# Performance work log

Measured on AMD Instinct MI355X. Metric: run time of the kernel, lower is better.

The kernel has to match this reference:

```python
import jax, jax.numpy as jnp
import numpy as np

HID, HEADS, HD = 512, 8, 64  # hid_dim, n_heads, head_dim
NEG = -1e10


def setup_inputs() -> dict:
    key = jax.random.key(0)
    ks = jax.random.split(key, 12)
    B, S = 4, 2048
    inp = {
        'query': jax.random.normal(ks[0], (B, S, HID), jnp.float32),
        'key': jax.random.normal(ks[1], (B, S, HID), jnp.float32),
        'value': jax.random.normal(ks[2], (B, S, HID), jnp.float32),
        'mask': jnp.ones((B, 1, 1, S), jnp.int32),
    }
    sc = 1.0 / np.sqrt(HID)
    for i, n in enumerate(['Wq', 'Wk', 'Wv', 'Wo']):
        inp[n] = jax.random.uniform(ks[3 + i], (HID, HID), jnp.float32, -sc, sc)
    for i, n in enumerate(['bq', 'bk', 'bv', 'bo']):
        inp[n] = jax.random.uniform(ks[7 + i], (HID,), jnp.float32, -sc, sc)
    return inp


def reference(query, key, value, mask, Wq, Wk, Wv, Wo, bq, bk, bv, bo):
    B = query.shape[0]

    def proj(x, W, b):
        # torch Linear: x @ W.T + b; then split heads -> [B, H, S, HD]
        y = jnp.einsum('bsd,ed->bse', x, W) + b
        return y.reshape(B, -1, HEADS, HD).transpose(0, 2, 1, 3)

    Q = proj(query, Wq, bq)
    K = proj(key, Wk, bk)
    V = proj(value, Wv, bv)
    scale = jnp.sqrt(jnp.float32(HD))
    E = jnp.einsum('bhqd,bhkd->bhqk', Q, K) / scale  # [B,H,Sq,Sk]
    E = jnp.where(mask == 0, NEG, E)
    A = jax.nn.softmax(E, axis=-1)  # dropout p=0 -> identity
    out = jnp.einsum('bhqk,bhkd->bhqd', A, V)
    out = out.transpose(0, 2, 1, 3).reshape(B, -1, HID)
    return jnp.einsum('bsd,ed->bse', out, Wo) + bo
```

## Files before the change

### kernel.cpp

```cpp
#include <hip/hip_runtime.h>
#include <hip/hip_bf16.h>


typedef __bf16 v8bf __attribute__((ext_vector_type(8)));
typedef __bf16 v4bf __attribute__((ext_vector_type(4)));
typedef float  v4f  __attribute__((ext_vector_type(4)));

#define MFMA16(a, b, c) __builtin_amdgcn_mfma_f32_16x16x32_bf16((a), (b), (c), 0, 0, 0)

__device__ __forceinline__ void gl16(const __bf16* g, __bf16* l) {
    __builtin_amdgcn_global_load_lds(
        (const __attribute__((address_space(1))) void*)g,
        (__attribute__((address_space(3))) void*)l, 16, 0, 0);
}

__device__ inline v8bf cvt8(const float* __restrict__ p) {
    const v4f f0 = *(const v4f*)p;
    const v4f f1 = *(const v4f*)(p + 4);
    v8bf r;
    r[0] = (__bf16)f0[0]; r[1] = (__bf16)f0[1]; r[2] = (__bf16)f0[2]; r[3] = (__bf16)f0[3];
    r[4] = (__bf16)f1[0]; r[5] = (__bf16)f1[1]; r[6] = (__bf16)f1[2]; r[7] = (__bf16)f1[3];
    return r;
}

__global__ __launch_bounds__(256) void cvt_all(
    const float* __restrict__ Wq, const float* __restrict__ Wk,
    const float* __restrict__ Wv, const float* __restrict__ Wo,
    const float* __restrict__ xq, const float* __restrict__ xk,
    const float* __restrict__ xv,
    __bf16* __restrict__ Wb, __bf16* __restrict__ xb)
{
    const int bid = blockIdx.x;
    if (bid < 1024) {
        const int idx = (bid * 256 + threadIdx.x) * 4;
        const int w = idx >> 18, off = idx & 262143;
        const float* src = (w == 0) ? Wq : (w == 1) ? Wk : (w == 2) ? Wv : Wo;
        const v4f x = *(const v4f*)(src + off);
        v4bf y;
        y[0] = (__bf16)x[0]; y[1] = (__bf16)x[1]; y[2] = (__bf16)x[2]; y[3] = (__bf16)x[3];
        *(v4bf*)(Wb + idx) = y;
    } else {
        const int idx = ((bid - 1024) * 256 + threadIdx.x) * 8;
        const int w = idx >> 22, off = idx & 4194303;
        const float* src = (w == 0) ? xq : (w == 1) ? xk : xv;
        *(v8bf*)(xb + idx) = cvt8(src + off);
    }
}

__global__ __launch_bounds__(256) void qkv_gemm(
    const __bf16* __restrict__ xb, const __bf16* __restrict__ Wb,
    const float* __restrict__ bq, const float* __restrict__ bk, const float* __restrict__ bv,
    __bf16* __restrict__ Qo, __bf16* __restrict__ Ko, __bf16* __restrict__ VTo)
{
    const int z = blockIdx.z;
    const __bf16* x    = xb + (size_t)z * 4194304;
    const __bf16* W    = Wb + (size_t)z * 262144;
    const float*  bias = (z == 0) ? bq : (z == 1) ? bk : bv;

    const int tid = threadIdx.x, wave = tid >> 6, lane = tid & 63;
    const int quad = lane >> 4, r = lane & 15;
    const int wm = wave >> 1, wn = wave & 1;
    const int row0 = blockIdx.x * 128, col0 = blockIdx.y * 128;

    __shared__ __align__(16) __bf16 As[2][4096];
    __shared__ __align__(16) __bf16 Bs[2][4096];

    const __bf16* aG[2];
    const __bf16* bG[2];
    int aOff[2];
    for (int j = 0; j < 2; j++) {
        const int s = wave * 2 + j;
        aG[j] = x + (size_t)(row0 + s * 16 + r) * 512 + quad * 8;
        bG[j] = W + (size_t)(col0 + s * 16 + r) * 512 + quad * 8;
        aOff[j] = s * 512;
    }

    v4f acc[4][4] = {};

    for (int j = 0; j < 2; j++) {
        gl16(aG[j], &As[0][aOff[j]]);
        gl16(bG[j], &Bs[0][aOff[j]]);
    }
    __syncthreads();

    for (int t = 0; t < 16; t++) {
        const int cur = t & 1;
        if (t < 15) {
            const int kk = (t + 1) * 32;
            for (int j = 0; j < 2; j++) {
                gl16(aG[j] + kk, &As[cur ^ 1][aOff[j]]);
                gl16(bG[j] + kk, &Bs[cur ^ 1][aOff[j]]);
            }
        }
        v8bf a[4], b[4];
        for (int i = 0; i < 4; i++)
            a[i] = ((const v8bf*)As[cur])[(wm * 4 + i) * 64 + lane];
        for (int i = 0; i < 4; i++)
            b[i] = ((const v8bf*)Bs[cur])[(wn * 4 + i) * 64 + lane];
        for (int mi = 0; mi < 4; mi++)
            for (int ni = 0; ni < 4; ni++)
                acc[mi][ni] = MFMA16(a[mi], b[ni], acc[mi][ni]);
        __syncthreads();
    }

    for (int ni = 0; ni < 4; ni++) {
        const int n = col0 + wn * 64 + ni * 16 + r;
        const float bv_ = bias[n];
        const int hh = n >> 6, hd = n & 63;
        for (int mi = 0; mi < 4; mi++) {
            const int mbase = row0 + wm * 64 + mi * 16 + quad * 4;
            const int bb = mbase >> 11, s0 = mbase & 2047;
            if (z == 2) {
                v4bf pk;
                for (int i = 0; i < 4; i++)
                    pk[i] = (__bf16)(acc[mi][ni][i] + bv_);
                *(v4bf*)&VTo[((size_t)((bb * 8 + hh) * 64 + hd)) * 2048 + s0] = pk;
            } else {
                __bf16* dst = (z == 0) ? Qo : Ko;
                for (int i = 0; i < 4; i++)
                    dst[((size_t)((bb * 8 + hh) * 2048 + s0 + i)) * 64 + hd] =
                        (__bf16)(acc[mi][ni][i] + bv_);
            }
        }
    }
}

__global__ __launch_bounds__(256, 4) void attn(
    const __bf16* __restrict__ Q, const __bf16* __restrict__ K,
    const __bf16* __restrict__ VT, const int* __restrict__ mask,
    float* __restrict__ P0, float* __restrict__ P1,
    float* __restrict__ L0, float* __restrict__ L1)
{
    const int id = blockIdx.y * 16 + blockIdx.x;
    const int x8 = id & 7, j = (id >> 3) & 3, qb = id >> 5;
    const int bh = x8 * 4 + j;
    const int b = bh >> 3, h = bh & 7;
    const int ks = blockIdx.z;
    float* __restrict__ Pp = ks ? P1 : P0;
    float* __restrict__ Lp = ks ? L1 : L0;
    const int tid = threadIdx.x, wave = tid >> 6, lane = tid & 63;
    const int quad = lane >> 4, r = lane & 15;
    const int q0 = qb * 128 + wave * 32;

    const __bf16* Qb = Q  + (size_t)bh * 2048 * 64;
    const __bf16* Kb = K  + (size_t)bh * 2048 * 64 + (size_t)ks * 1024 * 64;
    const __bf16* Vb = VT + (size_t)bh * 64 * 2048 + ks * 1024;
    const int*    mb = mask + (size_t)b * 2048 + ks * 1024;

    __shared__ __align__(16) __bf16 Kls[4096];
    __shared__ __align__(16) __bf16 Vls[4096];
    __shared__ __align__(16) float  biasF[1024];
    __shared__ __align__(16) __bf16 PF[4][4][64][8];

    for (int i = tid; i < 1024; i += 256)
        biasF[i] = (mb[i] != 0) ? 0.f : -1.0e10f;

    const int e1 = tid, e2 = tid + 256;
    int seg, l, t_, h_, rr, qd;
    seg = e1 >> 6; l = e1 & 63; t_ = seg >> 1; h_ = seg & 1; rr = l & 15; qd = l >> 4;
    const __bf16* kg1 = Kb + (size_t)(16 * t_ + rr) * 64   + h_ * 32 + qd * 8;
    const __bf16* vg1 = Vb + (size_t)(16 * t_ + rr) * 2048 + h_ * 32 + qd * 8;
    seg = e2 >> 6; l = e2 & 63; t_ = seg >> 1; h_ = seg & 1; rr = l & 15; qd = l >> 4;
    const __bf16* kg2 = Kb + (size_t)(16 * t_ + rr) * 64   + h_ * 32 + qd * 8;
    const __bf16* vg2 = Vb + (size_t)(16 * t_ + rr) * 2048 + h_ * 32 + qd * 8;

    v8bf qf[2][2];
    for (int g = 0; g < 2; g++) {
        qf[g][0] = *(const v8bf*)(Qb + (size_t)(q0 + g * 16 + r) * 64 +      quad * 8);
        qf[g][1] = *(const v8bf*)(Qb + (size_t)(q0 + g * 16 + r) * 64 + 32 + quad * 8);
    }

    v8bf ones;
    for (int i = 0; i < 8; i++) ones[i] = (__bf16)1.0f;

    v4f o[2][4] = {};
    v4f osum[2] = {};

    const float SC = 0.18033688f;

    const int entE = (quad >> 1) * 16 + r;
    const int entO = entE + 32;
    const int eoff = (quad & 1) * 4;

    v8bf ks1 = *(const v8bf*)kg1, ks2 = *(const v8bf*)kg2;
    v8bf vs1 = *(const v8bf*)vg1, vs2 = *(const v8bf*)vg2;

    for (int t = 0; t < 16; t++) {
        __syncthreads();
        ((v8bf*)Kls)[e1] = ks1; ((v8bf*)Kls)[e2] = ks2;
        ((v8bf*)Vls)[e1] = vs1; ((v8bf*)Vls)[e2] = vs2;
        __syncthreads();
        if (t < 15) {
            const int k0n = (t + 1) * 64;
            ks1 = *(const v8bf*)(kg1 + (size_t)k0n * 64);
            ks2 = *(const v8bf*)(kg2 + (size_t)k0n * 64);
            vs1 = *(const v8bf*)(vg1 + k0n);
            vs2 = *(const v8bf*)(vg2 + k0n);
        }
        const int k0 = t * 64;

        v4f sa[2][4] = {};
        for (int tt = 0; tt < 4; tt++) {
            const v8bf kf0 = ((const v8bf*)Kls)[(tt * 2 + 0) * 64 + lane];
            const v8bf kf1 = ((const v8bf*)Kls)[(tt * 2 + 1) * 64 + lane];
            sa[0][tt] = MFMA16(kf0, qf[0][0], sa[0][tt]);
            sa[0][tt] = MFMA16(kf1, qf[0][1], sa[0][tt]);
            sa[1][tt] = MFMA16(kf0, qf[1][0], sa[1][tt]);
            sa[1][tt] = MFMA16(kf1, qf[1][1], sa[1][tt]);
        }

        for (int tt = 0; tt < 4; tt++) {
            const v4f bl = *(const v4f*)&biasF[k0 + tt * 16 + quad * 4];
            const int ent = (tt & 1) ? entO : entE;
            const int pl = tt >> 1;
            for (int g = 0; g < 2; g++) {
                v4bf pk;
                for (int i = 0; i < 4; i++) {
                    const float p = __builtin_amdgcn_exp2f(fmaf(sa[g][tt][i], SC, bl[i]));
                    pk[i] = (__bf16)p;
                }
                *(v4bf*)&PF[wave][g * 2 + pl][ent][eoff] = pk;
            }
        }
        asm volatile("s_waitcnt lgkmcnt(0)" ::: "memory");
        v8bf pa[2][2];
        for (int g = 0; g < 2; g++) {
            pa[g][0] = *(const v8bf*)&PF[wave][g * 2 + 0][lane][0];
            pa[g][1] = *(const v8bf*)&PF[wave][g * 2 + 1][lane][0];
        }

        osum[0] = MFMA16(pa[0][0], ones, osum[0]);
        osum[0] = MFMA16(pa[0][1], ones, osum[0]);
        osum[1] = MFMA16(pa[1][0], ones, osum[1]);
        osum[1] = MFMA16(pa[1][1], ones, osum[1]);

        for (int t2 = 0; t2 < 4; t2++) {
            const v8bf vf0 = ((const v8bf*)Vls)[(t2 * 2 + 0) * 64 + lane];
            const v8bf vf1 = ((const v8bf*)Vls)[(t2 * 2 + 1) * 64 + lane];
            o[0][t2] = MFMA16(pa[0][0], vf0, o[0][t2]);
            o[0][t2] = MFMA16(pa[0][1], vf1, o[0][t2]);
            o[1][t2] = MFMA16(pa[1][0], vf0, o[1][t2]);
            o[1][t2] = MFMA16(pa[1][1], vf1, o[1][t2]);
        }
    }

    for (int g = 0; g < 2; g++) {
        if (r == 0)
            for (int i = 0; i < 4; i++)
                Lp[(size_t)bh * 2048 + q0 + g * 16 + quad * 4 + i] = osum[g][i];
        for (int t2 = 0; t2 < 4; t2++) {
            const int hd = t2 * 16 + r;
            for (int i = 0; i < 4; i++) {
                const int s = q0 + g * 16 + quad * 4 + i;
                Pp[((size_t)b * 2048 + s) * 512 + h * 64 + hd] = o[g][t2][i];
            }
        }
    }
}

__global__ __launch_bounds__(256) void combine(
    const float* __restrict__ P0, const float* __restrict__ P1,
    const float* __restrict__ L0, const float* __restrict__ L1,
    __bf16* __restrict__ AO)
{
    const size_t idx = ((size_t)blockIdx.x * 256 + threadIdx.x) * 8;
    const int bb = (int)(idx >> 20);
    const int rem = (int)(idx & 1048575);
    const int s = rem >> 9;
    const int h = (rem & 511) >> 6;
    const size_t li = ((size_t)bb * 8 + h) * 2048 + s;
    const float inv = 1.0f / (L0[li] + L1[li]);
    const v4f a0 = *(const v4f*)(P0 + idx), a1 = *(const v4f*)(P0 + idx + 4);
    const v4f b0 = *(const v4f*)(P1 + idx), b1 = *(const v4f*)(P1 + idx + 4);
    v8bf r;
    for (int i = 0; i < 4; i++) r[i]     = (__bf16)((a0[i] + b0[i]) * inv);
    for (int i = 0; i < 4; i++) r[i + 4] = (__bf16)((a1[i] + b1[i]) * inv);
    *(v8bf*)(AO + idx) = r;
}

__global__ __launch_bounds__(256) void out_gemm(
    const __bf16* __restrict__ Ai, const __bf16* __restrict__ W,
    const float* __restrict__ bias, float* __restrict__ y)
{
    const int tid = threadIdx.x, wave = tid >> 6, lane = tid & 63;
    const int quad = lane >> 4, r = lane & 15;
    const int wm = wave >> 1, wn = wave & 1;
    const int row0 = blockIdx.x * 64, col0 = blockIdx.y * 128;

    __shared__ __align__(16) __bf16 As[2][2048];
    __shared__ __align__(16) __bf16 Bs[2][4096];

    const __bf16* aG = Ai + (size_t)(row0 + wave * 16 + r) * 512 + quad * 8;
    const int aOff = wave * 512;
    const __bf16* bG[2];
    int bOff[2];
    for (int j = 0; j < 2; j++) {
        const int s = wave * 2 + j;
        bG[j] = W + (size_t)(col0 + s * 16 + r) * 512 + quad * 8;
        bOff[j] = s * 512;
    }

    v4f acc[2][4] = {};

    gl16(aG, &As[0][aOff]);
    gl16(bG[0], &Bs[0][bOff[0]]);
    gl16(bG[1], &Bs[0][bOff[1]]);
    __syncthreads();

    for (int t = 0; t < 16; t++) {
        const int cur = t & 1;
        if (t < 15) {
            const int kk = (t + 1) * 32;
            gl16(aG + kk, &As[cur ^ 1][aOff]);
            gl16(bG[0] + kk, &Bs[cur ^ 1][bOff[0]]);
            gl16(bG[1] + kk, &Bs[cur ^ 1][bOff[1]]);
        }
        v8bf a[2], b[4];
        for (int i = 0; i < 2; i++)
            a[i] = ((const v8bf*)As[cur])[(wm * 2 + i) * 64 + lane];
        for (int i = 0; i < 4; i++)
            b[i] = ((const v8bf*)Bs[cur])[(wn * 4 + i) * 64 + lane];
        for (int mi = 0; mi < 2; mi++)
            for (int ni = 0; ni < 4; ni++)
                acc[mi][ni] = MFMA16(a[mi], b[ni], acc[mi][ni]);
        __syncthreads();
    }

    for (int ni = 0; ni < 4; ni++) {
        const int n = col0 + wn * 64 + ni * 16 + r;
        const float bv_ = bias[n];
        for (int mi = 0; mi < 2; mi++) {
            const int mbase = row0 + wm * 32 + mi * 16 + quad * 4;
            for (int i = 0; i < 4; i++)
                y[(size_t)(mbase + i) * 512 + n] = acc[mi][ni][i] + bv_;
        }
    }
}

extern "C" void kernel_launch(void* const* d_in, const int* in_sizes, int n_in,
                              void* d_out, int out_size, void* d_ws, size_t ws_size,
                              hipStream_t stream)
{
    const float* q    = (const float*)d_in[0];
    const float* k    = (const float*)d_in[1];
    const float* v    = (const float*)d_in[2];
    const int*   mask = (const int*)d_in[3];
    const float* Wq   = (const float*)d_in[4];
    const float* Wk   = (const float*)d_in[5];
    const float* Wv   = (const float*)d_in[6];
    const float* Wo   = (const float*)d_in[7];
    const float* bq   = (const float*)d_in[8];
    const float* bk   = (const float*)d_in[9];
    const float* bv   = (const float*)d_in[10];
    const float* bo   = (const float*)d_in[11];

    __bf16* ws  = (__bf16*)d_ws;
    __bf16* Qw  = ws;
    __bf16* Kw  = ws + 4194304;
    __bf16* VTw = ws + 8388608;
    __bf16* Wb  = ws + 12582912;
    __bf16* xbw = ws + 13631488;
    float*  P0  = (float*)(ws + 13631488);
    float*  P1  = (float*)(ws + 22020096);
    float*  L0  = (float*)(ws + 30408704);
    float*  L1  = (float*)(ws + 30539776);
    __bf16* AOw = Qw;

    cvt_all<<<dim3(7168), 256, 0, stream>>>(Wq, Wk, Wv, Wo, q, k, v, Wb, xbw);
    qkv_gemm<<<dim3(64, 4, 3), 256, 0, stream>>>(xbw, Wb, bq, bk, bv, Qw, Kw, VTw);
    attn<<<dim3(16, 32, 2), 256, 0, stream>>>(Qw, Kw, VTw, mask, P0, P1, L0, L1);
    combine<<<dim3(2048), 256, 0, stream>>>(P0, P1, L0, L1, AOw);
    out_gemm<<<dim3(128, 4), 256, 0, stream>>>(AOw, Wb + 786432, bo, (float*)d_out);
}
```

Measured before the change: 208.1 us.

## Fuse fp32-to-bf16 activation conversion into QKV GEMM tile loads

The separate conversion pass over the query/key/value activations is removed. The QKV GEMM now loads fp32 activation tiles straight into LDS with global_load_lds and converts them to bf16 in registers before the MFMAs. This drops a full write and re-read of the bf16 activation copy, saving global memory traffic and part of a launch. In exchange the A-tile LDS footprint doubles (fp32), which may reduce occupancy, and each K-tile fetched by several column-blocks is converted redundantly.

```diff
diff --git a/kernel.cpp b/kernel.cpp
--- a/kernel.cpp
+++ b/kernel.cpp
@@ -8,52 +8,41 @@
 
 #define MFMA16(a, b, c) __builtin_amdgcn_mfma_f32_16x16x32_bf16((a), (b), (c), 0, 0, 0)
 
-__device__ __forceinline__ void gl16(const __bf16* g, __bf16* l) {
+__device__ __forceinline__ void gl16(const void* g, void* l) {
     __builtin_amdgcn_global_load_lds(
         (const __attribute__((address_space(1))) void*)g,
         (__attribute__((address_space(3))) void*)l, 16, 0, 0);
 }
 
-__device__ inline v8bf cvt8(const float* __restrict__ p) {
-    const v4f f0 = *(const v4f*)p;
-    const v4f f1 = *(const v4f*)(p + 4);
+__device__ __forceinline__ v8bf cvt8v(const v4f f0, const v4f f1) {
     v8bf r;
     r[0] = (__bf16)f0[0]; r[1] = (__bf16)f0[1]; r[2] = (__bf16)f0[2]; r[3] = (__bf16)f0[3];
     r[4] = (__bf16)f1[0]; r[5] = (__bf16)f1[1]; r[6] = (__bf16)f1[2]; r[7] = (__bf16)f1[3];
     return r;
 }
 
-__global__ __launch_bounds__(256) void cvt_all(
+__global__ __launch_bounds__(256) void cvt_w(
     const float* __restrict__ Wq, const float* __restrict__ Wk,
     const float* __restrict__ Wv, const float* __restrict__ Wo,
+    __bf16* __restrict__ out)
+{
+    const int idx = (blockIdx.x * 256 + threadIdx.x) * 4;
+    const int w = idx >> 18, off = idx & 262143;
+    const float* src = (w == 0) ? Wq : (w == 1) ? Wk : (w == 2) ? Wv : Wo;
+    const v4f x = *(const v4f*)(src + off);
+    v4bf y;
+    y[0] = (__bf16)x[0]; y[1] = (__bf16)x[1]; y[2] = (__bf16)x[2]; y[3] = (__bf16)x[3];
+    *(v4bf*)(out + idx) = y;
+}
+
+__global__ __launch_bounds__(256) void qkv_gemm(
     const float* __restrict__ xq, const float* __restrict__ xk,
-    const float* __restrict__ xv,
-    __bf16* __restrict__ Wb, __bf16* __restrict__ xb)
-{
-    const int bid = blockIdx.x;
-    if (bid < 1024) {
-        const int idx = (bid * 256 + threadIdx.x) * 4;
-        const int w = idx >> 18, off = idx & 262143;
-        const float* src = (w == 0) ? Wq : (w == 1) ? Wk : (w == 2) ? Wv : Wo;
-        const v4f x = *(const v4f*)(src + off);
-        v4bf y;
-        y[0] = (__bf16)x[0]; y[1] = (__bf16)x[1]; y[2] = (__bf16)x[2]; y[3] = (__bf16)x[3];
-        *(v4bf*)(Wb + idx) = y;
-    } else {
-        const int idx = ((bid - 1024) * 256 + threadIdx.x) * 8;
-        const int w = idx >> 22, off = idx & 4194303;
-        const float* src = (w == 0) ? xq : (w == 1) ? xk : xv;
-        *(v8bf*)(xb + idx) = cvt8(src + off);
-    }
-}
-
-__global__ __launch_bounds__(256) void qkv_gemm(
-    const __bf16* __restrict__ xb, const __bf16* __restrict__ Wb,
+    const float* __restrict__ xv, const __bf16* __restrict__ Wb,
     const float* __restrict__ bq, const float* __restrict__ bk, const float* __restrict__ bv,
     __bf16* __restrict__ Qo, __bf16* __restrict__ Ko, __bf16* __restrict__ VTo)
 {
     const int z = blockIdx.z;
-    const __bf16* x    = xb + (size_t)z * 4194304;
+    const float*  x    = (z == 0) ? xq : (z == 1) ? xk : xv;
     const __bf16* W    = Wb + (size_t)z * 262144;
     const float*  bias = (z == 0) ? bq : (z == 1) ? bk : bv;
 
@@ -62,39 +51,50 @@
     const int wm = wave >> 1, wn = wave & 1;
     const int row0 = blockIdx.x * 128, col0 = blockIdx.y * 128;
 
-    __shared__ __align__(16) __bf16 As[2][4096];
+    __shared__ __align__(16) float  Asf[2][4096];
     __shared__ __align__(16) __bf16 Bs[2][4096];
 
-    const __bf16* aG[2];
+    const float* aG[4];
+    int aOff[4];
+    for (int j = 0; j < 4; j++) {
+        const int s = wave * 4 + j;
+        aG[j] = x + (size_t)(row0 + (s >> 1) * 16 + r) * 512
+                  + (s & 1) * 16 + quad * 4;
+        aOff[j] = s * 256;
+    }
     const __bf16* bG[2];
-    int aOff[2];
+    int bOff[2];
     for (int j = 0; j < 2; j++) {
         const int s = wave * 2 + j;
-        aG[j] = x + (size_t)(row0 + s * 16 + r) * 512 + quad * 8;
         bG[j] = W + (size_t)(col0 + s * 16 + r) * 512 + quad * 8;
-        aOff[j] = s * 512;
+        bOff[j] = s * 512;
     }
 
     v4f acc[4][4] = {};
 
-    for (int j = 0; j < 2; j++) {
-        gl16(aG[j], &As[0][aOff[j]]);
-        gl16(bG[j], &Bs[0][aOff[j]]);
-    }
+    for (int j = 0; j < 4; j++) gl16(aG[j], &Asf[0][aOff[j]]);
+    gl16(bG[0], &Bs[0][bOff[0]]);
+    gl16(bG[1], &Bs[0][bOff[1]]);
     __syncthreads();
+
+    const int ch  = quad >> 1;
+    const int k0c = (quad & 1) * 2;
 
     for (int t = 0; t < 16; t++) {
         const int cur = t & 1;
         if (t < 15) {
             const int kk = (t + 1) * 32;
-            for (int j = 0; j < 2; j++) {
-                gl16(aG[j] + kk, &As[cur ^ 1][aOff[j]]);
-                gl16(bG[j] + kk, &Bs[cur ^ 1][aOff[j]]);
-            }
+            for (int j = 0; j < 4; j++) gl16(aG[j] + kk, &Asf[cur ^ 1][aOff[j]]);
+            gl16(bG[0] + kk, &Bs[cur ^ 1][bOff[0]]);
+            gl16(bG[1] + kk, &Bs[cur ^ 1][bOff[1]]);
         }
         v8bf a[4], b[4];
-        for (int i = 0; i < 4; i++)
-            a[i] = ((const v8bf*)As[cur])[(wm * 4 + i) * 64 + lane];
+        for (int i = 0; i < 4; i++) {
+            const int seg = (wm * 4 + i) * 2 + ch;
+            const v4f f0 = *(const v4f*)&Asf[cur][seg * 256 + (k0c * 16 + r) * 4];
+            const v4f f1 = *(const v4f*)&Asf[cur][seg * 256 + ((k0c + 1) * 16 + r) * 4];
+            a[i] = cvt8v(f0, f1);
+        }
         for (int i = 0; i < 4; i++)
             b[i] = ((const v8bf*)Bs[cur])[(wn * 4 + i) * 64 + lane];
         for (int mi = 0; mi < 4; mi++)
@@ -359,15 +359,14 @@
     __bf16* Kw  = ws + 4194304;
     __bf16* VTw = ws + 8388608;
     __bf16* Wb  = ws + 12582912;
-    __bf16* xbw = ws + 13631488;
     float*  P0  = (float*)(ws + 13631488);
     float*  P1  = (float*)(ws + 22020096);
     float*  L0  = (float*)(ws + 30408704);
     float*  L1  = (float*)(ws + 30539776);
     __bf16* AOw = Qw;
 
-    cvt_all<<<dim3(7168), 256, 0, stream>>>(Wq, Wk, Wv, Wo, q, k, v, Wb, xbw);
-    qkv_gemm<<<dim3(64, 4, 3), 256, 0, stream>>>(xbw, Wb, bq, bk, bv, Qw, Kw, VTw);
+    cvt_w<<<dim3(1024), 256, 0, stream>>>(Wq, Wk, Wv, Wo, Wb);
+    qkv_gemm<<<dim3(64, 4, 3), 256, 0, stream>>>(q, k, v, Wb, bq, bk, bv, Qw, Kw, VTw);
     attn<<<dim3(16, 32, 2), 256, 0, stream>>>(Qw, Kw, VTw, mask, P0, P1, L0, L1);
     combine<<<dim3(2048), 256, 0, stream>>>(P0, P1, L0, L1, AOw);
     out_gemm<<<dim3(128, 4), 256, 0, stream>>>(AOw, Wb + 786432, bo, (float*)d_out);
```

New measurement: 211.0 us. No clear change (+1.4%).
